# Kernel optimization log

Hardware: AMD Instinct MI355X
Metric: run time of the kernel (lower is better)

Reference implementation:

```python
import jax, jax.numpy as jnp
import numpy as np

HEAD_DIM = 64
N_HEADS = 16


def _rope_tables(seq_len, head_dim):
    pos = np.arange(seq_len, dtype=np.float32)
    freq = np.arange(0, head_dim, 2, dtype=np.float32) / head_dim
    inv_freq = 1.0 / (10000.0 ** freq)
    angles = np.outer(pos, inv_freq)                     # [S, D/2]
    angles = np.repeat(angles, 2, axis=-1)               # [S, D] interleaved
    return jnp.asarray(np.cos(angles)), jnp.asarray(np.sin(angles))


def _rotate_half(x):
    x1 = x[..., ::2]
    x2 = x[..., 1::2]
    return jnp.stack((-x2, x1), axis=-1).reshape(x.shape)


def _apply_rope(x, cos, sin):
    # x: [B, H, S, D]; cos/sin: [S, D]
    return x * cos + _rotate_half(x) * sin


def setup_inputs() -> dict:
    key = jax.random.key(0)
    ks = jax.random.split(key, 5)
    d = N_HEADS * HEAD_DIM
    B, S = 4, 2048
    s = 1.0 / np.sqrt(d)
    return {
        "x": jax.random.normal(ks[0], (B, S, d), dtype=jnp.float32),
        "Wq": jax.random.normal(ks[1], (d, d), dtype=jnp.float32) * s,
        "bq": jnp.zeros((d,), jnp.float32),
        "Wk": jax.random.normal(ks[2], (d, d), dtype=jnp.float32) * s,
        "bk": jnp.zeros((d,), jnp.float32),
        "Wv": jax.random.normal(ks[3], (d, d), dtype=jnp.float32) * s,
        "bv": jnp.zeros((d,), jnp.float32),
        "Wo": jax.random.normal(ks[4], (d, d), dtype=jnp.float32) * s,
        "bo": jnp.zeros((d,), jnp.float32),
    }


def reference(x, Wq, bq, Wk, bk, Wv, bv, Wo, bo):
    B, S, d = x.shape
    H, D = N_HEADS, HEAD_DIM
    scale = D ** -0.5

    q = (x @ Wq + bq).reshape(B, S, H, D).transpose(0, 2, 1, 3)  # [B,H,S,D]
    k = (x @ Wk + bk).reshape(B, S, H, D).transpose(0, 2, 1, 3)
    v = (x @ Wv + bv).reshape(B, S, H, D).transpose(0, 2, 1, 3)

    cos, sin = _rope_tables(S, D)
    q = _apply_rope(q, cos, sin)
    k = _apply_rope(k, cos, sin)

    att = jnp.einsum("bhqd,bhkd->bhqk", q, k) * scale            # [B,H,S,S]
    causal = jnp.tril(jnp.ones((S, S), dtype=bool))
    att = jnp.where(causal, att, -jnp.inf)
    att = jax.nn.softmax(att, axis=-1)

    y = jnp.einsum("bhqk,bhkd->bhqd", att, v)                    # [B,H,S,D]
    y = y.transpose(0, 2, 1, 3).reshape(B, S, d)
    return y @ Wo + bo
```

## Files before the change

### kernel.cpp

```cpp
#include <hip/hip_runtime.h>

typedef __bf16 bf16;
typedef __bf16 bf16x2 __attribute__((ext_vector_type(2)));
typedef __bf16 bf16x4 __attribute__((ext_vector_type(4)));
typedef __bf16 bf16x8 __attribute__((ext_vector_type(8)));
typedef float  f32x4  __attribute__((ext_vector_type(4)));

#define MFMA16(a,b,c) __builtin_amdgcn_mfma_f32_16x16x32_bf16(a,b,c,0,0,0)
#define GLL16(g, l) __builtin_amdgcn_global_load_lds( \
    (const __attribute__((address_space(1))) unsigned char*)(g), \
    (__attribute__((address_space(3))) unsigned char*)(l), 16, 0, 0)
#define BARRIER() asm volatile("s_barrier" ::: "memory")
#define DRAIN(n)  asm volatile("s_waitcnt vmcnt(" #n ")" ::: "memory")

constexpr int SEQ   = 2048;
constexpr int NH    = 16;
constexpr int HD    = 64;
constexpr int BATCH = 4;
constexpr int DM    = 1024;
constexpr int ROWS  = BATCH * SEQ;
constexpr size_t TEN = (size_t)BATCH * NH * SEQ * HD;

__global__ __launch_bounds__(256) void k_prep(const float* __restrict__ x,
                                              const float* __restrict__ W0,
                                              const float* __restrict__ W1,
                                              const float* __restrict__ W2,
                                              const float* __restrict__ W3,
                                              bf16* __restrict__ Wt_all,
                                              bf16* __restrict__ xb) {
    __shared__ float T[64][65];
    const int z = blockIdx.z;
    const int t = threadIdx.x;
    if (z == 4) {
        const int bi = blockIdx.y * 16 + blockIdx.x;
#pragma unroll
        for (int c = 0; c < 16; c++) {
            const size_t idx = (size_t)c * 524288 + ((size_t)bi * 256 + t) * 8;
            float4 f0 = *(const float4*)(x + idx);
            float4 f1 = *(const float4*)(x + idx + 4);
            bf16x8 o;
            o[0] = (bf16)f0.x; o[1] = (bf16)f0.y; o[2] = (bf16)f0.z; o[3] = (bf16)f0.w;
            o[4] = (bf16)f1.x; o[5] = (bf16)f1.y; o[6] = (bf16)f1.z; o[7] = (bf16)f1.w;
            *(bf16x8*)(xb + idx) = o;
        }
        return;
    }
    const float* W = (z == 0) ? W0 : (z == 1) ? W1 : (z == 2) ? W2 : W3;
    bf16* Wt = Wt_all + (size_t)z * DM * DM;
    const int kb = blockIdx.x, nb = blockIdx.y;
    const int rl = t >> 2, seg = t & 3;
    const float* src = W + (size_t)(kb * 64 + rl) * DM + nb * 64 + seg * 16;
#pragma unroll
    for (int j4 = 0; j4 < 4; j4++) {
        float4 f = *(const float4*)(src + j4 * 4);
        T[rl][seg * 16 + j4 * 4 + 0] = f.x;
        T[rl][seg * 16 + j4 * 4 + 1] = f.y;
        T[rl][seg * 16 + j4 * 4 + 2] = f.z;
        T[rl][seg * 16 + j4 * 4 + 3] = f.w;
    }
    __syncthreads();
    bf16* dst = Wt + (size_t)(nb * 64 + rl) * DM + kb * 64 + seg * 16;
    bf16x8 o0, o1;
#pragma unroll
    for (int j = 0; j < 8; j++) {
        o0[j] = (bf16)T[seg * 16 + j][rl];
        o1[j] = (bf16)T[seg * 16 + 8 + j][rl];
    }
    *(bf16x8*)dst = o0;
    *(bf16x8*)(dst + 8) = o1;
}

template <int MODE>
__global__ __launch_bounds__(256, 3) void k_gemm(const bf16* __restrict__ A,
                                                 const bf16* __restrict__ Wt0,
                                                 const float* __restrict__ b0,
                                                 const float* __restrict__ b1,
                                                 const float* __restrict__ b2,
                                                 bf16* __restrict__ vt,
                                                 void* __restrict__ out) {
    __shared__ __align__(1024) bf16 AsF[3][4096];
    __shared__ __align__(1024) bf16 BsF[3][4096];
    const int z = blockIdx.z;
    const bf16* Wt = Wt0 + (size_t)z * DM * DM;
    const float* bias = (z == 0) ? b0 : (z == 1) ? b1 : b2;

    const int t = threadIdx.x;
    const int w = t >> 6, lane = t & 63, quad = lane >> 4, l16 = lane & 15;
    const int bm = blockIdx.x * 128, bn = blockIdx.y * 128;
    const int wm = (w >> 1) * 64, wn = (w & 1) * 64;

    const int c0 = w * 2, c1 = w * 2 + 1;
    const int sg0 = c0 * 64 + lane, sg1 = c1 * 64 + lane;
    const int r0 = sg0 >> 2, r1 = sg1 >> 2;
    const int csg0 = (sg0 & 3) ^ ((r0 >> 1) & 3);
    const int csg1 = (sg1 & 3) ^ ((r1 >> 1) & 3);
    const bf16* gA0 = A  + (size_t)(bm + r0) * DM + csg0 * 8;
    const bf16* gA1 = A  + (size_t)(bm + r1) * DM + csg1 * 8;
    const bf16* gB0 = Wt + (size_t)(bn + r0) * DM + csg0 * 8;
    const bf16* gB1 = Wt + (size_t)(bn + r1) * DM + csg1 * 8;

#define STG(buf, tt) do { \
    GLL16(gA0 + (size_t)(tt) * 32, &AsF[buf][c0 * 512]); \
    GLL16(gA1 + (size_t)(tt) * 32, &AsF[buf][c1 * 512]); \
    GLL16(gB0 + (size_t)(tt) * 32, &BsF[buf][c0 * 512]); \
    GLL16(gB1 + (size_t)(tt) * 32, &BsF[buf][c1 * 512]); \
} while (0)

    STG(0, 0);
    STG(1, 1);

    int offA[4], offB[4];
#pragma unroll
    for (int mt = 0; mt < 4; mt++) {
        const int r = wm + mt * 16 + l16;
        offA[mt] = r * 32 + ((quad ^ ((r >> 1) & 3)) << 3);
    }
#pragma unroll
    for (int nt = 0; nt < 4; nt++) {
        const int r = wn + nt * 16 + l16;
        offB[nt] = r * 32 + ((quad ^ ((r >> 1) & 3)) << 3);
    }

    f32x4 zero = {0.f, 0.f, 0.f, 0.f};
    f32x4 acc[4][4];
#pragma unroll
    for (int mt = 0; mt < 4; mt++)
#pragma unroll
        for (int nt = 0; nt < 4; nt++) acc[mt][nt] = zero;

    DRAIN(4);
    BARRIER();

#pragma unroll
    for (int tk = 0; tk < 32; tk++) {
        const int cur = tk % 3;
        if (tk < 31) {
            const int nb = (tk + 2) % 3;
            const int ts = (tk + 2 > 31) ? 31 : (tk + 2);
            STG(nb, ts);
        }
        const bf16* ab = &AsF[cur][0];
        const bf16* bb = &BsF[cur][0];
        bf16x8 af[4], bfr[4];
#pragma unroll
        for (int mt = 0; mt < 4; mt++) af[mt]  = *(const bf16x8*)(ab + offA[mt]);
#pragma unroll
        for (int nt = 0; nt < 4; nt++) bfr[nt] = *(const bf16x8*)(bb + offB[nt]);
#pragma unroll
        for (int mt = 0; mt < 4; mt++)
#pragma unroll
            for (int nt = 0; nt < 4; nt++)
                acc[mt][nt] = MFMA16(af[mt], bfr[nt], acc[mt][nt]);
        if (tk < 31) {
            DRAIN(4);
            BARRIER();
        }
    }
#undef STG

    float bv[4], invf[4];
#pragma unroll
    for (int nt = 0; nt < 4; nt++) {
        const int col = bn + wn + nt * 16 + l16;
        bv[nt] = bias[col];
        if (MODE == 0) {
            const int i = (col & 63) >> 1;
            invf[nt] = __builtin_exp2f(-0.41524101186092029f * (float)i);
        }
    }
    const int odd = l16 & 1;

    if (MODE == 0 && z == 2) {
#pragma unroll
        for (int mt = 0; mt < 4; mt++) {
            const int row0 = bm + wm + mt * 16 + quad * 4;
            const int b = row0 >> 11, s0 = row0 & (SEQ - 1);
#pragma unroll
            for (int nt = 0; nt < 4; nt++) {
                const int col = bn + wn + nt * 16 + l16;
                const int h = col >> 6, dd = col & 63;
                bf16x4 o;
#pragma unroll
                for (int rg = 0; rg < 4; rg++) o[rg] = (bf16)(acc[mt][nt][rg] + bv[nt]);
                *(bf16x4*)(vt + ((size_t)((b * NH + h) * HD + dd)) * SEQ + s0) = o;
            }
        }
        return;
    }

#pragma unroll
    for (int mt = 0; mt < 4; mt++) {
#pragma unroll
        for (int nt = 0; nt < 4; nt++) {
            const int col = bn + wn + nt * 16 + l16;
#pragma unroll
            for (int rg = 0; rg < 4; rg++) {
                const int row = bm + wm + mt * 16 + quad * 4 + rg;
                float val = acc[mt][nt][rg] + bv[nt];
                if (MODE == 0) {
                    const int b = row >> 11, s = row & (SEQ - 1);
                    const int h = col >> 6, dd = col & 63;
                    const float partner = __shfl_xor(val, 1);
                    float sn, cs;
                    __sincosf((float)s * invf[nt], &sn, &cs);
                    val = odd ? (val * cs + partner * sn)
                              : (val * cs - partner * sn);
                    if (z == 0) val *= 0.125f;
                    ((bf16*)out)[(size_t)z * TEN +
                                 (((size_t)(b * NH + h)) * SEQ + s) * HD + dd] = (bf16)val;
                } else {
                    ((float*)out)[(size_t)row * DM + col] = val;
                }
            }
        }
    }
}

__global__ __launch_bounds__(256, 2) void k_attn(const bf16* __restrict__ q,
                                                 const bf16* __restrict__ k,
                                                 const bf16* __restrict__ vt,
                                                 bf16* __restrict__ y) {
    __shared__ __align__(1024) bf16 KsF[3][4096];
    __shared__ __align__(1024) bf16 VsF[3][4096];
    __shared__ __align__(1024) bf16 PsF[4 * 32 * 64];
    const int t = threadIdx.x;
    const int w = t >> 6, lane = t & 63, quad = lane >> 4, l16 = lane & 15;
    const int bh = blockIdx.x;
    const int qb = 15 - (int)blockIdx.y;
    const int b = bh >> 4, h = bh & 15;

    const int srow = lane >> 3;
    const int gseg = (lane & 7) ^ srow;
    const int c0 = w, c1 = w + 4;

    const bf16* kbase = k  + (size_t)bh * SEQ * HD;
    const bf16* vbase = vt + (size_t)bh * HD * SEQ;
    const float NEG_INF = -__builtin_inff();

    const int koff0 = (c0 * 8 + srow) * HD + gseg * 8;
    const int koff1 = (c1 * 8 + srow) * HD + gseg * 8;
    const int voff0 = (c0 * 8 + srow) * SEQ + gseg * 8;
    const int voff1 = (c1 * 8 + srow) * SEQ + gseg * 8;

#define STGKV(buf, tt) do { \
    GLL16(kbase + (size_t)(tt) * 64 * HD + koff0, &KsF[buf][c0 * 512]); \
    GLL16(kbase + (size_t)(tt) * 64 * HD + koff1, &KsF[buf][c1 * 512]); \
    GLL16(vbase + (size_t)(tt) * 64 + voff0, &VsF[buf][c0 * 512]); \
    GLL16(vbase + (size_t)(tt) * 64 + voff1, &VsF[buf][c1 * 512]); \
} while (0)

    bf16x8 qf[2][2];
#pragma unroll
    for (int mt = 0; mt < 2; mt++) {
        const bf16* qrow = q + ((size_t)bh * SEQ + qb * 128 + w * 32 + mt * 16 + l16) * HD;
        qf[mt][0] = *(const bf16x8*)(qrow + quad * 8);
        qf[mt][1] = *(const bf16x8*)(qrow + 32 + quad * 8);
    }

    const int ktmax = 2 * qb + 1;
    STGKV(0, 0);
    STGKV(1, 1);

    int off_kv[4][2];
#pragma unroll
    for (int nt = 0; nt < 4; nt++) {
        const int r = nt * 16 + l16;
#pragma unroll
        for (int hh = 0; hh < 2; hh++) {
            const int sg = hh * 4 + quad;
            off_kv[nt][hh] = r * 64 + ((sg ^ (r & 7)) << 3);
        }
    }
    const bf16 *pf_p[2][2];
#pragma unroll
    for (int mt = 0; mt < 2; mt++) {
        const int r = mt * 16 + l16;
#pragma unroll
        for (int hh = 0; hh < 2; hh++) {
            const int sg = hh * 4 + quad;
            pf_p[mt][hh] = PsF + w * 2048 + r * 64 + ((sg ^ (r & 7)) << 3);
        }
    }

    f32x4 zero = {0.f, 0.f, 0.f, 0.f};
    f32x4 minus10 = {-10.f, -10.f, -10.f, -10.f};
    f32x4 acc_o[2][4];
    float l_acc[2][4];
#pragma unroll
    for (int mt = 0; mt < 2; mt++)
#pragma unroll
        for (int nt = 0; nt < 4; nt++) acc_o[mt][nt] = zero;
#pragma unroll
    for (int mt = 0; mt < 2; mt++)
#pragma unroll
        for (int rg = 0; rg < 4; rg++) l_acc[mt][rg] = 0.f;

    DRAIN(4);
    BARRIER();

    int cur = 0, nb = 2;
    for (int kt = 0; kt <= ktmax; kt++) {
        if (kt < ktmax) {
            const int ts = (kt + 2 > ktmax) ? ktmax : (kt + 2);
            STGKV(nb, ts);
        }
        const bf16* kb_ = &KsF[0][0] + cur * 4096;
        const bf16* vb_ = &VsF[0][0] + cur * 4096;

        const int d = qb * 128 + w * 32 - kt * 64;
        if (d > -32) {
            f32x4 accs[2][4];
#pragma unroll
            for (int nt = 0; nt < 4; nt++) {
                const bf16x8 kf0 = *(const bf16x8*)(kb_ + off_kv[nt][0]);
                const bf16x8 kf1 = *(const bf16x8*)(kb_ + off_kv[nt][1]);
#pragma unroll
                for (int mt = 0; mt < 2; mt++) {
                    f32x4 a = minus10;
                    a = MFMA16(qf[mt][0], kf0, a);
                    a = MFMA16(qf[mt][1], kf1, a);
                    accs[mt][nt] = a;
                }
            }
            if (d < 64) {
#pragma unroll
                for (int mt = 0; mt < 2; mt++) {
                    const int qr = d + mt * 16 + quad * 4;
#pragma unroll
                    for (int nt = 0; nt < 4; nt++) {
                        const int kv = nt * 16 + l16;
#pragma unroll
                        for (int rg = 0; rg < 4; rg++)
                            if (kv > qr + rg) accs[mt][nt][rg] = NEG_INF;
                    }
                }
            }
#pragma unroll
            for (int mt = 0; mt < 2; mt++) {
#pragma unroll
                for (int nt = 0; nt < 4; nt++) {
#pragma unroll
                    for (int rg = 0; rg < 4; rg++) {
                        const float p = __expf(accs[mt][nt][rg]);
                        l_acc[mt][rg] += p;
                        const int prow = mt * 16 + quad * 4 + rg;
                        const int psg  = (nt * 2 + (l16 >> 3)) ^ (prow & 7);
                        PsF[w * 2048 + prow * 64 + psg * 8 + (l16 & 7)] = (bf16)p;
                    }
                }
            }
            bf16x8 pf[2][2];
#pragma unroll
            for (int mt = 0; mt < 2; mt++) {
                pf[mt][0] = *(const bf16x8*)pf_p[mt][0];
                pf[mt][1] = *(const bf16x8*)pf_p[mt][1];
            }
#pragma unroll
            for (int nt = 0; nt < 4; nt++) {
                const bf16x8 vf0 = *(const bf16x8*)(vb_ + off_kv[nt][0]);
                const bf16x8 vf1 = *(const bf16x8*)(vb_ + off_kv[nt][1]);
#pragma unroll
                for (int mt = 0; mt < 2; mt++) {
                    acc_o[mt][nt] = MFMA16(pf[mt][0], vf0, acc_o[mt][nt]);
                    acc_o[mt][nt] = MFMA16(pf[mt][1], vf1, acc_o[mt][nt]);
                }
            }
        }
        if (kt < ktmax) {
            DRAIN(4);
            BARRIER();
        }
        cur = (cur == 2) ? 0 : cur + 1;
        nb  = (nb  == 2) ? 0 : nb  + 1;
    }
#undef STGKV

#pragma unroll
    for (int mt = 0; mt < 2; mt++) {
#pragma unroll
        for (int rg = 0; rg < 4; rg++) {
            float rs = l_acc[mt][rg];
            rs += __shfl_xor(rs, 1);
            rs += __shfl_xor(rs, 2);
            rs += __shfl_xor(rs, 4);
            rs += __shfl_xor(rs, 8);
            const float inv = 1.0f / rs;
            const int s = qb * 128 + w * 32 + mt * 16 + quad * 4 + rg;
#pragma unroll
            for (int nt = 0; nt < 4; nt++) {
                const float val = acc_o[mt][nt][rg] * inv;
                y[((size_t)(b * SEQ + s)) * DM + h * HD + nt * 16 + l16] = (bf16)val;
            }
        }
    }
}

extern "C" void kernel_launch(void* const* d_in, const int* in_sizes, int n_in,
                              void* d_out, int out_size, void* d_ws, size_t ws_size,
                              hipStream_t stream) {
    const float* x  = (const float*)d_in[0];
    const float* Wq = (const float*)d_in[1];
    const float* bq = (const float*)d_in[2];
    const float* Wk = (const float*)d_in[3];
    const float* bk = (const float*)d_in[4];
    const float* Wv = (const float*)d_in[5];
    const float* bv = (const float*)d_in[6];
    const float* Wo = (const float*)d_in[7];
    const float* bo = (const float*)d_in[8];

    char* ws = (char*)d_ws;
    bf16* xb   = (bf16*)(ws);
    bf16* wall = (bf16*)(ws + (16ull << 20));
    bf16* qb   = (bf16*)(ws + (24ull << 20));
    bf16* kb   = (bf16*)(ws + (40ull << 20));
    bf16* vtb  = (bf16*)(ws + (72ull << 20));
    bf16* wot  = wall + 3ull * DM * DM;

    k_prep<<<dim3(16, 16, 5), 256, 0, stream>>>(x, Wq, Wk, Wv, Wo, wall, xb);
    k_gemm<0><<<dim3(64, 8, 3), 256, 0, stream>>>(xb, wall, bq, bk, bv, vtb, qb);
    k_attn<<<dim3(64, 16), 256, 0, stream>>>(qb, kb, vtb, xb);
    k_gemm<1><<<dim3(64, 8, 1), 256, 0, stream>>>(xb, wot, bo, bo, bo, vtb, d_out);
}
```

Before: 253.7 us.

## Restructure projection GEMM to 256x128 tiles with 512 threads and K=64 stages

```diff
diff --git a/kernel.cpp b/kernel.cpp
--- a/kernel.cpp
+++ b/kernel.cpp
@@ -18,7 +18,6 @@
 constexpr int HD    = 64;
 constexpr int BATCH = 4;
 constexpr int DM    = 1024;
-constexpr int ROWS  = BATCH * SEQ;
 constexpr size_t TEN = (size_t)BATCH * NH * SEQ * HD;
 
 __global__ __launch_bounds__(256) void k_prep(const float* __restrict__ x,
@@ -71,112 +70,128 @@
 }
 
 template <int MODE>
-__global__ __launch_bounds__(256, 3) void k_gemm(const bf16* __restrict__ A,
+__global__ __launch_bounds__(512, 1) void k_gemm(const bf16* __restrict__ A,
                                                  const bf16* __restrict__ Wt0,
                                                  const float* __restrict__ b0,
                                                  const float* __restrict__ b1,
                                                  const float* __restrict__ b2,
                                                  bf16* __restrict__ vt,
                                                  void* __restrict__ out) {
-    __shared__ __align__(1024) bf16 AsF[3][4096];
-    __shared__ __align__(1024) bf16 BsF[3][4096];
-    const int z = blockIdx.z;
+    __shared__ __align__(1024) bf16 LA[3][16384];
+    __shared__ __align__(1024) bf16 LB[2][8192];
+    const int t = threadIdx.x;
+    const int w = t >> 6, lane = t & 63, quad = lane >> 4, l16 = lane & 15;
+    const int bm = blockIdx.x * 256;
+    const int by = blockIdx.y;
+    const int z  = (MODE == 0) ? (by >> 3) : 0;
+    const int bn = (MODE == 0) ? ((by & 7) * 128) : (by * 128);
     const bf16* Wt = Wt0 + (size_t)z * DM * DM;
     const float* bias = (z == 0) ? b0 : (z == 1) ? b1 : b2;
-
-    const int t = threadIdx.x;
-    const int w = t >> 6, lane = t & 63, quad = lane >> 4, l16 = lane & 15;
-    const int bm = blockIdx.x * 128, bn = blockIdx.y * 128;
-    const int wm = (w >> 1) * 64, wn = (w & 1) * 64;
-
-    const int c0 = w * 2, c1 = w * 2 + 1;
-    const int sg0 = c0 * 64 + lane, sg1 = c1 * 64 + lane;
-    const int r0 = sg0 >> 2, r1 = sg1 >> 2;
-    const int csg0 = (sg0 & 3) ^ ((r0 >> 1) & 3);
-    const int csg1 = (sg1 & 3) ^ ((r1 >> 1) & 3);
-    const bf16* gA0 = A  + (size_t)(bm + r0) * DM + csg0 * 8;
-    const bf16* gA1 = A  + (size_t)(bm + r1) * DM + csg1 * 8;
-    const bf16* gB0 = Wt + (size_t)(bn + r0) * DM + csg0 * 8;
-    const bf16* gB1 = Wt + (size_t)(bn + r1) * DM + csg1 * 8;
-
-#define STG(buf, tt) do { \
-    GLL16(gA0 + (size_t)(tt) * 32, &AsF[buf][c0 * 512]); \
-    GLL16(gA1 + (size_t)(tt) * 32, &AsF[buf][c1 * 512]); \
-    GLL16(gB0 + (size_t)(tt) * 32, &BsF[buf][c0 * 512]); \
-    GLL16(gB1 + (size_t)(tt) * 32, &BsF[buf][c1 * 512]); \
+    const int wm = (w >> 2) * 128, wn = (w & 3) * 32;
+
+    const int srow = lane >> 3;
+    const int sseg = (lane & 7) ^ srow;
+    const bf16* gA = A  + (size_t)(bm + w * 8 + srow) * DM + sseg * 8;
+    const bf16* gB = Wt + (size_t)(bn + w * 8 + srow) * DM + sseg * 8;
+
+#define STGA_P(lp, tt, c) do { \
+    const bf16* _g = gA + (size_t)(c) * 128 * DM + (size_t)(tt) * 64; \
+    bf16* _l = (lp) + ((c) * 16 + w) * 512; \
+    GLL16(_g, _l); GLL16(_g + 64 * DM, _l + 4096); \
 } while (0)
-
-    STG(0, 0);
-    STG(1, 1);
-
-    int offA[4], offB[4];
-#pragma unroll
-    for (int mt = 0; mt < 4; mt++) {
-        const int r = wm + mt * 16 + l16;
-        offA[mt] = r * 32 + ((quad ^ ((r >> 1) & 3)) << 3);
-    }
-#pragma unroll
-    for (int nt = 0; nt < 4; nt++) {
-        const int r = wn + nt * 16 + l16;
-        offB[nt] = r * 32 + ((quad ^ ((r >> 1) & 3)) << 3);
-    }
+#define STGB_P(lp, tt) do { \
+    const bf16* _g = gB + (size_t)(tt) * 64; \
+    bf16* _l = (lp) + w * 512; \
+    GLL16(_g, _l); GLL16(_g + 64 * DM, _l + 4096); \
+} while (0)
+
+    const int sA0 = (quad ^ (l16 & 7)) << 3;
+    const int sA1 = ((4 + quad) ^ (l16 & 7)) << 3;
 
     f32x4 zero = {0.f, 0.f, 0.f, 0.f};
-    f32x4 acc[4][4];
-#pragma unroll
-    for (int mt = 0; mt < 4; mt++)
-#pragma unroll
-        for (int nt = 0; nt < 4; nt++) acc[mt][nt] = zero;
-
-    DRAIN(4);
+    f32x4 acc[8][2];
+#pragma unroll
+    for (int mt = 0; mt < 8; mt++)
+#pragma unroll
+        for (int nt = 0; nt < 2; nt++) acc[mt][nt] = zero;
+    bf16x8 bfr[2][2];
+
+#define PH(la_, lb_, mb, READB, STAGE_STMT, DRAIN_STMT) do { \
+    const bf16* _la = (la_); \
+    if (READB) { \
+        const bf16* _lb = (lb_); \
+        _Pragma("unroll") \
+        for (int nt = 0; nt < 2; nt++) { \
+            const int r = (wn + nt * 16 + l16) * 64; \
+            bfr[nt][0] = *(const bf16x8*)(_lb + r + sA0); \
+            bfr[nt][1] = *(const bf16x8*)(_lb + r + sA1); \
+        } \
+    } \
+    bf16x8 af[4][2]; \
+    _Pragma("unroll") \
+    for (int mi = 0; mi < 4; mi++) { \
+        const int r = (wm + ((mb) + mi) * 16 + l16) * 64; \
+        af[mi][0] = *(const bf16x8*)(_la + r + sA0); \
+        af[mi][1] = *(const bf16x8*)(_la + r + sA1); \
+    } \
+    STAGE_STMT; \
+    DRAIN_STMT; \
+    BARRIER(); \
+    __builtin_amdgcn_s_setprio(1); \
+    _Pragma("unroll") \
+    for (int mi = 0; mi < 4; mi++) \
+        _Pragma("unroll") \
+        for (int nt = 0; nt < 2; nt++) { \
+            f32x4 a = acc[(mb) + mi][nt]; \
+            a = MFMA16(af[mi][0], bfr[nt][0], a); \
+            a = MFMA16(af[mi][1], bfr[nt][1], a); \
+            acc[(mb) + mi][nt] = a; \
+        } \
+    __builtin_amdgcn_s_setprio(0); \
+    BARRIER(); \
+} while (0)
+
+    STGA_P(&LA[0][0], 0, 0); STGA_P(&LA[0][0], 0, 1); STGB_P(&LB[0][0], 0);
+    STGA_P(&LA[1][0], 1, 0); STGA_P(&LA[1][0], 1, 1); STGB_P(&LB[1][0], 1);
+    DRAIN(6);
     BARRIER();
 
-#pragma unroll
-    for (int tk = 0; tk < 32; tk++) {
-        const int cur = tk % 3;
-        if (tk < 31) {
-            const int nb = (tk + 2) % 3;
-            const int ts = (tk + 2 > 31) ? 31 : (tk + 2);
-            STG(nb, ts);
-        }
-        const bf16* ab = &AsF[cur][0];
-        const bf16* bb = &BsF[cur][0];
-        bf16x8 af[4], bfr[4];
-#pragma unroll
-        for (int mt = 0; mt < 4; mt++) af[mt]  = *(const bf16x8*)(ab + offA[mt]);
-#pragma unroll
-        for (int nt = 0; nt < 4; nt++) bfr[nt] = *(const bf16x8*)(bb + offB[nt]);
-#pragma unroll
-        for (int mt = 0; mt < 4; mt++)
-#pragma unroll
-            for (int nt = 0; nt < 4; nt++)
-                acc[mt][nt] = MFMA16(af[mt], bfr[nt], acc[mt][nt]);
-        if (tk < 31) {
-            DRAIN(4);
-            BARRIER();
-        }
-    }
-#undef STG
-
-    float bv[4], invf[4];
-#pragma unroll
-    for (int nt = 0; nt < 4; nt++) {
+    int ae = 0, ao = 1, an = 2;
+    for (int i = 0; i < 8; i++) {
+        const int tE = (i < 7) ? 2 * i + 2 : 15;
+        const int tO = (i < 7) ? 2 * i + 3 : 15;
+        bf16* lae = &LA[0][0] + ae * 16384;
+        bf16* lao = &LA[0][0] + ao * 16384;
+        bf16* lan = &LA[0][0] + an * 16384;
+        PH(lae, &LB[0][0], 0, 1, { STGA_P(lan, tE, 0); STGA_P(lan, tE, 1); }, );
+        PH(lae, (const bf16*)0, 4, 0, STGB_P(&LB[0][0], tE), DRAIN(6));
+        PH(lao, &LB[1][0], 0, 1, { STGA_P(lae, tO, 0); STGA_P(lae, tO, 1); }, );
+        PH(lao, (const bf16*)0, 4, 0, STGB_P(&LB[1][0], tO), DRAIN(6));
+        const int tmp = ae; ae = an; an = ao; ao = tmp;
+    }
+#undef PH
+#undef STGA_P
+#undef STGB_P
+
+    float bv[2], invf[2];
+#pragma unroll
+    for (int nt = 0; nt < 2; nt++) {
         const int col = bn + wn + nt * 16 + l16;
         bv[nt] = bias[col];
         if (MODE == 0) {
-            const int i = (col & 63) >> 1;
-            invf[nt] = __builtin_exp2f(-0.41524101186092029f * (float)i);
+            const int ip = (col & 63) >> 1;
+            invf[nt] = __builtin_exp2f(-0.41524101186092029f * (float)ip);
         }
     }
     const int odd = l16 & 1;
 
     if (MODE == 0 && z == 2) {
 #pragma unroll
-        for (int mt = 0; mt < 4; mt++) {
+        for (int mt = 0; mt < 8; mt++) {
             const int row0 = bm + wm + mt * 16 + quad * 4;
             const int b = row0 >> 11, s0 = row0 & (SEQ - 1);
 #pragma unroll
-            for (int nt = 0; nt < 4; nt++) {
+            for (int nt = 0; nt < 2; nt++) {
                 const int col = bn + wn + nt * 16 + l16;
                 const int h = col >> 6, dd = col & 63;
                 bf16x4 o;
@@ -189,9 +204,9 @@
     }
 
 #pragma unroll
-    for (int mt = 0; mt < 4; mt++) {
-#pragma unroll
-        for (int nt = 0; nt < 4; nt++) {
+    for (int mt = 0; mt < 8; mt++) {
+#pragma unroll
+        for (int nt = 0; nt < 2; nt++) {
             const int col = bn + wn + nt * 16 + l16;
 #pragma unroll
             for (int rg = 0; rg < 4; rg++) {
@@ -417,7 +432,7 @@
     bf16* wot  = wall + 3ull * DM * DM;
 
     k_prep<<<dim3(16, 16, 5), 256, 0, stream>>>(x, Wq, Wk, Wv, Wo, wall, xb);
-    k_gemm<0><<<dim3(64, 8, 3), 256, 0, stream>>>(xb, wall, bq, bk, bv, vtb, qb);
+    k_gemm<0><<<dim3(32, 24), 512, 0, stream>>>(xb, wall, bq, bk, bv, vtb, qb);
     k_attn<<<dim3(64, 16), 256, 0, stream>>>(qb, kb, vtb, xb);
-    k_gemm<1><<<dim3(64, 8, 1), 256, 0, stream>>>(xb, wot, bo, bo, bo, vtb, d_out);
+    k_gemm<1><<<dim3(32, 8), 512, 0, stream>>>(xb, wot, bo, bo, bo, vtb, d_out);
 }
```

After: 250.7 us. Within noise of the previous version (-1.2%).
